# Kernel tuning notes

Hardware: AMD Instinct MI355X
Metric: run time of the kernel (lower is better)

Reference implementation:

```python
import jax, jax.numpy as jnp
import numpy as np

B, T, HID = 2, 1024, 2048
H, DK, DV = 16, 128, 128
KC = 4          # short-conv kernel size
CHUNK = 64
EPS = 1e-5


def _dwconv_silu(x, w):
    # causal depthwise conv1d + SiLU: x [B,T,C], w [C,K]
    K = w.shape[1]
    xp = jnp.pad(x, ((0, 0), (K - 1, 0), (0, 0)))
    y = sum(xp[:, i:i + x.shape[1], :] * w[:, i] for i in range(K))
    return jax.nn.silu(y)


def _l2norm(x):
    return x * jax.lax.rsqrt(jnp.sum(x * x, -1, keepdims=True) + 1e-6)


def setup_inputs() -> dict:
    key = jax.random.key(0)
    ks = jax.random.split(key, 22)
    std = 0.02
    w = lambda k, s: jax.random.normal(k, s, jnp.float32) * std
    return dict(
        hidden_states=jax.random.normal(ks[0], (B, T, HID), jnp.float32),
        Wq=w(ks[1], (HID, H * DK)),
        Wk=w(ks[2], (HID, H * DK)),
        Wv=w(ks[3], (HID, H * DV)),
        conv_wq=w(ks[4], (H * DK, KC)),
        conv_wk=w(ks[5], (H * DK, KC)),
        conv_wv=w(ks[6], (H * DV, KC)),
        Wgb1=w(ks[7], (HID, DV)), Wgb2=w(ks[8], (DV, H * DK)),
        Wgd1=w(ks[9], (HID, DV)), Wgd2=w(ks[10], (DV, H * DK)),
        Wbb=w(ks[11], (HID, H)), Wbd=w(ks[12], (HID, H)),
        Wlam=w(ks[13], (HID, H)),
        A_log=jnp.log(jax.random.uniform(ks[14], (H,), jnp.float32, 1.0, 16.0)),
        dt_bias=jnp.zeros((H * DK,), jnp.float32),
        Wg1=w(ks[15], (HID, DV)), Wg2=w(ks[16], (DV, H * DV)),
        bg2=jnp.zeros((H * DV,), jnp.float32),
        onorm_w=jnp.ones((DV,), jnp.float32),
        Wo=w(ks[17], (H * DV, HID)),
    )


def _fkda_core(q, k, v, gf, gs, bf, bs):
    # dual-state (fast/slow) gated delta rule.
    # q,k: [B,T,H,DK]; v: [B,T,H,DV]; gf/gs: log-decay [B,T,H,DK]; bf/bs: [B,T,H]
    scale = DK ** -0.5
    tm = lambda x: jnp.moveaxis(x, 1, 0)                 # time-major
    qT, kT, vT = tm(q) * scale, tm(k), tm(v)
    g2 = jnp.stack([tm(gf), tm(gs)], 1)                  # [T,2,B,H,DK]
    b2 = jnp.stack([tm(bf), tm(bs)], 1)                  # [T,2,B,H]
    NC = T // CHUNK
    chunkify = lambda x: x.reshape((NC, CHUNK) + x.shape[1:])
    inputs = tuple(map(chunkify, (qT, kT, vT, g2, b2)))

    def step(S, inp):
        qt, kt, vt, gt, bt = inp                         # S: [2,B,H,DK,DV]
        S = S * jnp.exp(gt)[..., None]                   # per-channel decay on key dim
        mem = jnp.einsum('bhk,sbhkv->sbhv', kt, S)       # current memory readout
        u = bt[..., None] * (vt[None] - mem)             # delta-rule residual write
        S = S + jnp.einsum('bhk,sbhv->sbhkv', kt, u)
        o = jnp.einsum('bhk,sbhkv->sbhv', qt, S)
        return S, o

    @jax.checkpoint
    def chunk_step(S, inp):
        return jax.lax.scan(step, S, inp)

    S0 = jnp.zeros((2, q.shape[0], H, DK, DV), q.dtype)
    _, o = jax.lax.scan(chunk_step, S0, inputs)          # [NC,CHUNK,2,B,H,DV]
    o = o.reshape((T,) + o.shape[2:])
    return jnp.moveaxis(o[:, 0], 0, 1), jnp.moveaxis(o[:, 1], 0, 1)


def reference(hidden_states, Wq, Wk, Wv, conv_wq, conv_wk, conv_wv,
              Wgb1, Wgb2, Wgd1, Wgd2, Wbb, Wbd, Wlam, A_log, dt_bias,
              Wg1, Wg2, bg2, onorm_w, Wo):
    x = hidden_states
    b, t, _ = x.shape
    q = _dwconv_silu(x @ Wq, conv_wq).reshape(b, t, H, DK)
    k = _dwconv_silu(x @ Wk, conv_wk).reshape(b, t, H, DK)
    v = _dwconv_silu(x @ Wv, conv_wv).reshape(b, t, H, DV)
    g_base = ((x @ Wgb1) @ Wgb2).reshape(b, t, H, DK)    # low-rank decay gates
    g_delta = ((x @ Wgd1) @ Wgd2).reshape(b, t, H, DK)
    bb, bd = x @ Wbb, x @ Wbd
    lam = jax.nn.sigmoid(x @ Wlam)                       # [b,t,H] fast/slow mix
    beta_fast = jax.nn.sigmoid(bb + bd)
    beta_slow = jax.nn.sigmoid(bb - bd)
    dtb = dt_bias.reshape(H, DK)
    gate_of = lambda g: -jnp.exp(A_log)[None, None, :, None] * jax.nn.softplus(g + dtb)
    gf = gate_of(g_base + g_delta)                       # fused_kda_gate, fast
    gs = gate_of(g_base - g_delta)                       # slow (share_decay_gate=False)
    q, k = _l2norm(q), _l2norm(k)                        # use_qk_l2norm_in_kernel
    o_f, o_s = _fkda_core(q, k, v, gf, gs, beta_fast, beta_slow)
    o = lam[..., None] * o_f + (1.0 - lam[..., None]) * o_s
    gate = ((x @ Wg1) @ Wg2 + bg2).reshape(b, t, H, DV)
    o = o * jax.lax.rsqrt(jnp.mean(o * o, -1, keepdims=True) + EPS) * onorm_w
    o = o * jax.nn.sigmoid(gate)                         # FusedRMSNormGated(sigmoid)
    return o.reshape(b, t, H * DV) @ Wo
```

## Files before the change

### kernel.cpp

```cpp
#include <hip/hip_runtime.h>
#include <hip/hip_bf16.h>
#include <math.h>
#include <stdint.h>

#define B_   2
#define T_   1024
#define HID_ 2048
#define H_   16
#define DK_  128
#define DV_  128
#define TS_  16

typedef __bf16 bf16;
typedef __attribute__((ext_vector_type(8))) __bf16 bf16x8;
typedef __attribute__((ext_vector_type(4))) float f32x4;

typedef __attribute__((address_space(3))) uint32_t* lds_ptr_t;
typedef const __attribute__((address_space(1))) uint32_t* glb_ptr_t;

__device__ __forceinline__ float sigmoidf_(float x) {
    return 1.0f / (1.0f + __expf(-x));
}

__device__ __forceinline__ void ldg_to_lds16(const void* g, void* lds) {
    __builtin_amdgcn_global_load_lds((glb_ptr_t)(uintptr_t)g,
                                     (lds_ptr_t)(uintptr_t)lds, 16, 0, 0);
}

template <int CTRL>
__device__ __forceinline__ float dpp_ror_add(float x) {
    int yi = __builtin_amdgcn_update_dpp(
        0, __builtin_bit_cast(int, x), CTRL, 0xF, 0xF, true);
    return x + __builtin_bit_cast(float, yi);
}
__device__ __forceinline__ float row16_allreduce(float x) {
    x = dpp_ror_add<0x128>(x);
    x = dpp_ror_add<0x124>(x);
    x = dpp_ror_add<0x122>(x);
    x = dpp_ror_add<0x121>(x);
    return x;
}

__global__ __launch_bounds__(256) void cast_bf16_kernel(
    const float* __restrict__ in, bf16* __restrict__ out)
{
    int i = blockIdx.x * 256 + threadIdx.x;
    float4 a = ((const float4*)in)[2 * i];
    float4 b = ((const float4*)in)[2 * i + 1];
    bf16x8 o;
    o[0] = (bf16)a.x; o[1] = (bf16)a.y; o[2] = (bf16)a.z; o[3] = (bf16)a.w;
    o[4] = (bf16)b.x; o[5] = (bf16)b.y; o[6] = (bf16)b.z; o[7] = (bf16)b.w;
    ((bf16x8*)out)[i] = o;
}

__global__ __launch_bounds__(256) void tcast_kernel(
    const float* __restrict__ W, bf16* __restrict__ Wt, int K, int N)
{
    __shared__ float tile[32][33];
    const int k0 = blockIdx.y * 32, n0 = blockIdx.x * 32;
    const int r = threadIdx.x >> 5, c = threadIdx.x & 31;
    #pragma unroll
    for (int i = 0; i < 4; ++i)
        tile[r + 8 * i][c] = W[(size_t)(k0 + r + 8 * i) * N + n0 + c];
    __syncthreads();
    #pragma unroll
    for (int i = 0; i < 4; ++i)
        Wt[(size_t)(n0 + r + 8 * i) * K + k0 + c] = (bf16)tile[c][r + 8 * i];
}

__global__ __launch_bounds__(256) void tcast_off_kernel(
    const float* __restrict__ W, bf16* __restrict__ Wt,
    int N, int noff, int koff, float sign)
{
    __shared__ float tile[32][33];
    const int k0 = blockIdx.y * 32, n0 = blockIdx.x * 32;
    const int r = threadIdx.x >> 5, c = threadIdx.x & 31;
    #pragma unroll
    for (int i = 0; i < 4; ++i)
        tile[r + 8 * i][c] = W[(size_t)(k0 + r + 8 * i) * N + n0 + c];
    __syncthreads();
    #pragma unroll
    for (int i = 0; i < 4; ++i)
        Wt[(size_t)(noff + n0 + r + 8 * i) * 256 + koff + k0 + c] =
            (bf16)(sign * tile[c][r + 8 * i]);
}

__global__ __launch_bounds__(256) void mfma_gemm_kernel(
    const bf16* __restrict__ A, const bf16* __restrict__ Bt,
    const float* __restrict__ bias, void* __restrict__ Cout,
    int M, int N, int Kfull, int lda, int ldc, int bf16out)
{
    __shared__ bf16 As[128 * 32];
    __shared__ bf16 Bs[128 * 32];

    const int tid  = threadIdx.x;
    const int w    = tid >> 6;
    const int lane = tid & 63;
    const int n0   = blockIdx.x * 128;
    const int m0   = blockIdx.y * 128;
    const int wm   = (w >> 1) * 64;
    const int wn   = (w & 1) * 64;

    const int lr = lane >> 2;
    const int lc = (lane & 3) * 8;

    f32x4 acc[4][4];
    #pragma unroll
    for (int i = 0; i < 4; ++i)
        #pragma unroll
        for (int j = 0; j < 4; ++j) acc[i][j] = (f32x4)0.0f;

    const bf16* ApL = As + (wm + (lane & 15)) * 32 + (lane >> 4) * 8;
    const bf16* BpL = Bs + (wn + (lane & 15)) * 32 + (lane >> 4) * 8;

    for (int k0 = 0; k0 < Kfull; k0 += 32) {
        #pragma unroll
        for (int i = 0; i < 2; ++i) {
            const int rr = (w * 2 + i) * 16 + lr;
            ldg_to_lds16(A  + (size_t)(m0 + rr) * lda   + k0 + lc, As + (w * 2 + i) * 512);
            ldg_to_lds16(Bt + (size_t)(n0 + rr) * Kfull + k0 + lc, Bs + (w * 2 + i) * 512);
        }
        __syncthreads();

        bf16x8 af[4], bfr[4];
        #pragma unroll
        for (int i = 0; i < 4; ++i) af[i]  = *(const bf16x8*)(ApL + i * 16 * 32);
        #pragma unroll
        for (int j = 0; j < 4; ++j) bfr[j] = *(const bf16x8*)(BpL + j * 16 * 32);
        #pragma unroll
        for (int i = 0; i < 4; ++i)
            #pragma unroll
            for (int j = 0; j < 4; ++j)
                acc[i][j] = __builtin_amdgcn_mfma_f32_16x16x32_bf16(
                    af[i], bfr[j], acc[i][j], 0, 0, 0);
        __syncthreads();
    }

    #pragma unroll
    for (int i = 0; i < 4; ++i) {
        const int row = m0 + wm + i * 16 + (lane >> 4) * 4;
        #pragma unroll
        for (int j = 0; j < 4; ++j) {
            const int col = n0 + wn + j * 16 + (lane & 15);
            const float bv = bias ? bias[col] : 0.0f;
            #pragma unroll
            for (int r = 0; r < 4; ++r) {
                float v = acc[i][j][r] + bv;
                if (bf16out) ((bf16*)Cout)[(size_t)(row + r) * ldc + col] = (bf16)v;
                else ((float*)Cout)[(size_t)(row + r) * ldc + col] = v;
            }
        }
    }
}

__global__ __launch_bounds__(256) void midcast_kernel(
    const float* __restrict__ src, bf16* __restrict__ midb)
{
    int i = blockIdx.x * 256 + threadIdx.x;
    int m = i / 96, c4 = i - m * 96;
    float4 v = *(const float4*)(src + (size_t)m * 6528 + 6144 + c4 * 4);
    bf16 o[4] = {(bf16)v.x, (bf16)v.y, (bf16)v.z, (bf16)v.w};
    *(uint64_t*)(midb + (size_t)m * 384 + c4 * 4) = *(uint64_t*)o;
}

__global__ __launch_bounds__(256) void skinny3_kernel(
    const float* __restrict__ x, const float* __restrict__ Wbb,
    const float* __restrict__ Wbd, const float* __restrict__ Wlam,
    float* __restrict__ bb, float* __restrict__ bd, float* __restrict__ lam)
{
    __shared__ float xs[16][128];
    __shared__ float wsh[128][48];
    const int m0  = blockIdx.x * 16;
    const int tid = threadIdx.x;
    const int r = tid >> 4, cg = tid & 15;
    float acc0 = 0.f, acc1 = 0.f, acc2 = 0.f;

    for (int k0 = 0; k0 < HID_; k0 += 128) {
        __syncthreads();
        #pragma unroll
        for (int i = 0; i < 2; ++i) {
            int f = tid + 256 * i;
            int rr = f >> 5, cc = (f & 31) * 4;
            *(float4*)&xs[rr][cc] = *(const float4*)(x + (size_t)(m0 + rr) * HID_ + k0 + cc);
        }
        #pragma unroll
        for (int i = 0; i < 2; ++i) {
            int f = tid + 256 * i;
            int kk = f >> 2, cc = (f & 3) * 4;
            *(float4*)&wsh[kk][cc]      = *(const float4*)(Wbb  + (size_t)(k0 + kk) * 16 + cc);
            *(float4*)&wsh[kk][16 + cc] = *(const float4*)(Wbd  + (size_t)(k0 + kk) * 16 + cc);
            *(float4*)&wsh[kk][32 + cc] = *(const float4*)(Wlam + (size_t)(k0 + kk) * 16 + cc);
        }
        __syncthreads();
        #pragma unroll 8
        for (int kk = 0; kk < 128; ++kk) {
            float xv = xs[r][kk];
            acc0 += xv * wsh[kk][cg];
            acc1 += xv * wsh[kk][16 + cg];
            acc2 += xv * wsh[kk][32 + cg];
        }
    }
    size_t o = (size_t)(m0 + r) * 16 + cg;
    bb[o] = acc0; bd[o] = acc1; lam[o] = acc2;
}

__global__ __launch_bounds__(256) void conv_silu_kernel(
    const float* __restrict__ xin, int ldx, int coloff,
    const float* __restrict__ w, float* __restrict__ yout, int mode)
{
    const int bt  = blockIdx.x;
    const int t   = bt & (T_ - 1);
    const int tid = threadIdx.x;
    const float* xr = xin + (size_t)bt * ldx + coloff;

    float val[8];
    #pragma unroll
    for (int jj = 0; jj < 8; ++jj) {
        int c = tid + 256 * jj;
        float4 wc = *(const float4*)(w + (size_t)c * 4);
        const float* xc = xr + c;
        float acc = wc.w * xc[0];
        if (t >= 1) acc += wc.z * xc[-ldx];
        if (t >= 2) acc += wc.y * xc[-2 * ldx];
        if (t >= 3) acc += wc.x * xc[-3 * ldx];
        val[jj] = acc * sigmoidf_(acc);
    }

    if (mode > 0) {
        __shared__ float red[4][8];
        const int wv = tid >> 6;
        #pragma unroll
        for (int jj = 0; jj < 8; ++jj) {
            float v2 = val[jj] * val[jj];
            #pragma unroll
            for (int m = 1; m < 64; m <<= 1) v2 += __shfl_xor(v2, m);
            if ((tid & 63) == 0) red[wv][jj] = v2;
        }
        __syncthreads();
        const int wb = (tid >> 7) * 2;
        #pragma unroll
        for (int jj = 0; jj < 8; ++jj) {
            float ss = red[wb][jj] + red[wb + 1][jj];
            float sc = rsqrtf(ss + 1e-6f);
            if (mode == 2) sc *= 0.08838834764831845f;
            val[jj] *= sc;
        }
    }

    const size_t row = (size_t)bt * HID_;
    #pragma unroll
    for (int jj = 0; jj < 8; ++jj)
        yout[row + tid + 256 * jj] = val[jj];
}

__global__ __launch_bounds__(256) void decay_gate_kernel(
    float* gfgs, const float* __restrict__ A_log,
    const float* __restrict__ dt_bias)
{
    size_t i = (size_t)blockIdx.x * 256 + threadIdx.x;
    int c = (int)(i & (HID_ - 1));
    size_t m = i >> 11;
    int h = c >> 7;
    float* pf = gfgs + m * 4096 + c;
    float* ps = pf + 2048;
    float na = -__expf(A_log[h]);
    float db = dt_bias[c];
    float xf = *pf + db;
    float xs = *ps + db;
    float spf = (xf > 20.0f) ? xf : log1pf(__expf(xf));
    float sps = (xs > 20.0f) ? xs : log1pf(__expf(xs));
    *pf = __expf(na * spf);
    *ps = __expf(na * sps);
}

__global__ __launch_bounds__(256) void fkda_kernel(
    const float* __restrict__ qp, const float* __restrict__ kp,
    const float* __restrict__ vp, const float* __restrict__ egf,
    const float* __restrict__ egs, int ldeg,
    const float* __restrict__ bbp, const float* __restrict__ bdp,
    float* __restrict__ ofp, float* __restrict__ osp)
{
    const int bx = blockIdx.x;
    const int bh = bx & 31;
    const int sv = bx >> 5;
    const int b  = bh >> 4;
    const int h  = bh & 15;
    const int s  = sv >> 3;
    const int vc = sv & 7;

    const float* eg = s ? egs : egf;
    float*       op = s ? osp : ofp;
    const float  bsign = s ? -1.0f : 1.0f;

    const int tid  = threadIdx.x;
    const int lane = tid & 63;
    const int w    = tid >> 6;
    const int kseg = lane & 15;
    const int colb = w * 4 + (lane >> 4);

    const size_t base  = (size_t)b * T_ * HID_ + (size_t)h * DK_;
    const size_t baseg = (size_t)b * T_ * ldeg + (size_t)h * DK_;

    __shared__ float EG[TS_ * 128];
    __shared__ float KK[TS_ * 128];
    __shared__ float QQ[TS_ * 128];
    __shared__ float VV[TS_ * 16];
    __shared__ float OT[TS_ * 16];
    __shared__ float BT[TS_];

    float S[8];
    #pragma unroll
    for (int j = 0; j < 8; ++j) S[j] = 0.0f;

    const int l5  = lane & 31;
    const int ttl = lane >> 5;
    const int cg  = (l5 < 16) ? (l5 * 8) : ((l5 - 16) * 8 + 4);
    const int sl  = kseg * 4;

    for (int t0 = 0; t0 < T_; t0 += TS_) {
        #pragma unroll
        for (int i = 0; i < 2; ++i) {
            int n  = w * 2 + i;
            int tt = n * 2 + ttl;
            size_t rq = base  + (size_t)(t0 + tt) * HID_ + cg;
            size_t rg = baseg + (size_t)(t0 + tt) * ldeg + cg;
            ldg_to_lds16(eg + rg, EG + n * 256);
            ldg_to_lds16(kp + rq, KK + n * 256);
            ldg_to_lds16(qp + rq, QQ + n * 256);
        }
        if (tid < 64) {
            int tt = tid >> 2, vo = (tid & 3) * 4;
            size_t g = base + (size_t)(t0 + tt) * HID_ + vc * 16 + vo;
            ((float4*)VV)[tid] = *(const float4*)(vp + g);
        }
        if (tid < TS_) {
            size_t gi = ((size_t)b * T_ + t0 + tid) * H_ + h;
            BT[tid] = sigmoidf_(bbp[gi] + bsign * bdp[gi]);
        }
        __syncthreads();

        #pragma unroll
        for (int tt = 0; tt < TS_; ++tt) {
            float e[8], kf[8], qf[8];
            *(float4*)&e[0]  = *(const float4*)(EG + tt * 128 + sl);
            *(float4*)&e[4]  = *(const float4*)(EG + tt * 128 + 64 + sl);
            *(float4*)&kf[0] = *(const float4*)(KK + tt * 128 + sl);
            *(float4*)&kf[4] = *(const float4*)(KK + tt * 128 + 64 + sl);
            *(float4*)&qf[0] = *(const float4*)(QQ + tt * 128 + sl);
            *(float4*)&qf[4] = *(const float4*)(QQ + tt * 128 + 64 + sl);
            float vcol = VV[tt * 16 + colb];
            float btv  = BT[tt];

            float p0 = 0.0f, p1 = 0.0f;
            #pragma unroll
            for (int j = 0; j < 8; j += 2) {
                S[j]     *= e[j];     p0 += kf[j]     * S[j];
                S[j + 1] *= e[j + 1]; p1 += kf[j + 1] * S[j + 1];
            }
            float p = row16_allreduce(p0 + p1);

            float u = btv * (vcol - p);

            float o0 = 0.0f, o1 = 0.0f;
            #pragma unroll
            for (int j = 0; j < 8; j += 2) {
                S[j]     += kf[j]     * u; o0 += qf[j]     * S[j];
                S[j + 1] += kf[j + 1] * u; o1 += qf[j + 1] * S[j + 1];
            }
            float oo = row16_allreduce(o0 + o1);

            if (kseg == 0) OT[tt * 16 + colb] = oo;
        }
        __syncthreads();

        if (tid < 64) {
            int tt = tid >> 2, vo = (tid & 3) * 4;
            size_t g = base + (size_t)(t0 + tt) * HID_ + vc * 16 + vo;
            *(float4*)(op + g) = ((const float4*)OT)[tid];
        }
    }
}

__global__ __launch_bounds__(256) void mix_norm_gate_kernel(
    const float* of, const float* os, const float* lam_pre,
    const float* gate, const float* onorm_w, bf16* outp)
{
    const int bt  = blockIdx.x;
    const int tid = threadIdx.x;
    const size_t row = (size_t)bt * HID_;

    float val[8];
    #pragma unroll
    for (int jj = 0; jj < 8; ++jj) {
        int c = tid + 256 * jj;
        int h = c >> 7;
        float l = sigmoidf_(lam_pre[(size_t)bt * H_ + h]);
        val[jj] = l * of[row + c] + (1.0f - l) * os[row + c];
    }

    __shared__ float red[4][8];
    const int wv = tid >> 6;
    #pragma unroll
    for (int jj = 0; jj < 8; ++jj) {
        float v2 = val[jj] * val[jj];
        #pragma unroll
        for (int m = 1; m < 64; m <<= 1) v2 += __shfl_xor(v2, m);
        if ((tid & 63) == 0) red[wv][jj] = v2;
    }
    __syncthreads();
    const int wb = (tid >> 7) * 2;
    #pragma unroll
    for (int jj = 0; jj < 8; ++jj) {
        int c = tid + 256 * jj;
        float ss   = red[wb][jj] + red[wb + 1][jj];
        float mean = ss * (1.0f / 128.0f);
        float sc   = rsqrtf(mean + 1e-5f) * onorm_w[c & 127];
        float g    = sigmoidf_(gate[row + c]);
        outp[row + c] = (bf16)(val[jj] * sc * g);
    }
}

extern "C" void kernel_launch(void* const* d_in, const int* in_sizes, int n_in,
                              void* d_out, int out_size, void* d_ws, size_t ws_size,
                              hipStream_t stream) {
    const float* x       = (const float*)d_in[0];
    const float* Wq      = (const float*)d_in[1];
    const float* Wk      = (const float*)d_in[2];
    const float* Wv      = (const float*)d_in[3];
    const float* conv_wq = (const float*)d_in[4];
    const float* conv_wk = (const float*)d_in[5];
    const float* conv_wv = (const float*)d_in[6];
    const float* Wgb1    = (const float*)d_in[7];
    const float* Wgb2    = (const float*)d_in[8];
    const float* Wgd1    = (const float*)d_in[9];
    const float* Wgd2    = (const float*)d_in[10];
    const float* Wbb     = (const float*)d_in[11];
    const float* Wbd     = (const float*)d_in[12];
    const float* Wlam    = (const float*)d_in[13];
    const float* A_log   = (const float*)d_in[14];
    const float* dt_bias = (const float*)d_in[15];
    const float* Wg1     = (const float*)d_in[16];
    const float* Wg2     = (const float*)d_in[17];
    const float* bg2     = (const float*)d_in[18];
    const float* onorm_w = (const float*)d_in[19];
    const float* Wo      = (const float*)d_in[20];
    float* out = (float*)d_out;

    const size_t M = (size_t)B_ * T_;

    float* ws = (float*)d_ws;
    size_t off = 0;
    auto alloc = [&](size_t nfloats) { float* p = ws + off; off += nfloats; return p; };

    float* bufQKV = alloc(M * 6528);
    float* wqkvTf = alloc((size_t)6528 * HID_ / 2);
    float* xbf    = alloc(M * HID_ / 2);
    float* bufQ   = alloc(M * HID_);
    float* bufK   = alloc(M * HID_);
    float* bufV   = alloc(M * HID_);
    float* bufC   = alloc(M * HID_);
    float* bufD   = alloc(M * HID_);
    float* midbf  = alloc(M * 384 / 2);
    float* bb     = alloc(M * H_);
    float* bd     = alloc(M * H_);
    float* lamp   = alloc(M * H_);

    bf16* xb    = (bf16*)xbf;
    bf16* obf   = (bf16*)xbf;
    bf16* wqkvT = (bf16*)wqkvTf;
    bf16* woT   = wqkvT;
    bf16* wcat  = wqkvT + (size_t)HID_ * HID_;
    bf16* wgate = wcat + (size_t)4096 * 256;
    bf16* midb  = (bf16*)midbf;
    float* gfgs = bufQKV;
    float* bufE = bufQKV + M * 4096;

    dim3 blk(256);
    auto gemm = [&](const bf16* A, const bf16* Bt, const float* bias, void* C,
                    int Mm, int Nn, int Kk, int lda, int ldc, int bf16out) {
        dim3 grid(Nn / 128, Mm / 128);
        mfma_gemm_kernel<<<grid, blk, 0, stream>>>(A, Bt, bias, C, Mm, Nn, Kk,
                                                   lda, ldc, bf16out);
    };
    auto tcast = [&](const float* W, bf16* Wt, int Kk, int Nn) {
        tcast_kernel<<<dim3(Nn / 32, Kk / 32), blk, 0, stream>>>(W, Wt, Kk, Nn);
    };

    cast_bf16_kernel<<<dim3((unsigned)(M * HID_ / 8 / 256)), blk, 0, stream>>>(x, xb);

    tcast(Wq,   wqkvT,                          HID_, HID_);
    tcast(Wk,   wqkvT + (size_t)2048 * HID_,    HID_, HID_);
    tcast(Wv,   wqkvT + (size_t)4096 * HID_,    HID_, HID_);
    tcast(Wgb1, wqkvT + (size_t)6144 * HID_,    HID_, 128);
    tcast(Wgd1, wqkvT + (size_t)6272 * HID_,    HID_, 128);
    tcast(Wg1,  wqkvT + (size_t)6400 * HID_,    HID_, 128);
    gemm(xb, wqkvT, nullptr, bufQKV, (int)M, 6528, HID_, HID_, 6528, 0);

    conv_silu_kernel<<<dim3(B_ * T_), blk, 0, stream>>>(bufQKV, 6528, 0,
        conv_wq, bufQ, 2);
    conv_silu_kernel<<<dim3(B_ * T_), blk, 0, stream>>>(bufQKV, 6528, 2048,
        conv_wk, bufK, 1);
    conv_silu_kernel<<<dim3(B_ * T_), blk, 0, stream>>>(bufQKV, 6528, 4096,
        conv_wv, bufV, 0);

    midcast_kernel<<<dim3((unsigned)(M * 96 / 256)), blk, 0, stream>>>(bufQKV, midb);

    skinny3_kernel<<<dim3((unsigned)(M / 16)), blk, 0, stream>>>(
        x, Wbb, Wbd, Wlam, bb, bd, lamp);

    tcast_off_kernel<<<dim3(64, 4), blk, 0, stream>>>(Wgb2, wcat, HID_, 0,    0,   1.0f);
    tcast_off_kernel<<<dim3(64, 4), blk, 0, stream>>>(Wgd2, wcat, HID_, 0,    128, 1.0f);
    tcast_off_kernel<<<dim3(64, 4), blk, 0, stream>>>(Wgb2, wcat, HID_, 2048, 0,   1.0f);
    tcast_off_kernel<<<dim3(64, 4), blk, 0, stream>>>(Wgd2, wcat, HID_, 2048, 128, -1.0f);
    tcast(Wg2, wgate, 128, HID_);
    tcast(Wo,  woT,   HID_, HID_);
    gemm(midb,       wcat,  nullptr, gfgs, (int)M, 4096, 256, 384, 4096, 0);
    gemm(midb + 256, wgate, bg2,     bufE, (int)M, HID_, 128, 384, HID_, 0);

    decay_gate_kernel<<<dim3((unsigned)(M * HID_ / 256)), blk, 0, stream>>>(
        gfgs, A_log, dt_bias);

    fkda_kernel<<<dim3(512), blk, 0, stream>>>(bufQ, bufK, bufV,
        gfgs, gfgs + 2048, 4096, bb, bd, bufC, bufD);

    mix_norm_gate_kernel<<<dim3(B_ * T_), blk, 0, stream>>>(
        bufC, bufD, lamp, bufE, onorm_w, obf);

    gemm(obf, woT, nullptr, out, (int)M, HID_, HID_, HID_, HID_, 0);
}
```

Measured before the change: 751.1 us.

## Fuse weight casts, conv launches and decay gate; store intermediates in bf16

Merges the many transpose-cast launches into a few batched grids and the three conv launches into one 2D grid. The decay-gate softplus/exp is folded into the GEMM epilogue, and the midcast pass is dropped because the GEMM output is now written as bf16. Q, K and the gate are stored as bf16, and the recurrence kernel loads bf16 Q/K into shared memory. This reduces launch count and memory traffic, at the cost of lower precision for the QKV projection outputs ahead of the conv.

```diff
diff --git a/kernel.cpp b/kernel.cpp
--- a/kernel.cpp
+++ b/kernel.cpp
@@ -53,42 +53,74 @@
     ((bf16x8*)out)[i] = o;
 }
 
-__global__ __launch_bounds__(256) void tcast_kernel(
-    const float* __restrict__ W, bf16* __restrict__ Wt, int K, int N)
-{
+__device__ __forceinline__ void tcast_body(
+    const float* __restrict__ W, bf16* __restrict__ Wt, int K, int N,
+    int bx, int by, float sign)
+{
+    __shared__ float tile[32][33];
+    const int k0 = by * 32, n0 = bx * 32;
+    const int r = threadIdx.x >> 5, c = threadIdx.x & 31;
+    #pragma unroll
+    for (int i = 0; i < 4; ++i)
+        tile[r + 8 * i][c] = W[(size_t)(k0 + r + 8 * i) * N + n0 + c];
+    __syncthreads();
+    #pragma unroll
+    for (int i = 0; i < 4; ++i)
+        Wt[(size_t)(n0 + r + 8 * i) * K + k0 + c] =
+            (bf16)(sign * tile[c][r + 8 * i]);
+}
+
+__global__ __launch_bounds__(256) void tcast4_kernel(
+    const float* Wq, const float* Wk, const float* Wv, const float* Wo,
+    bf16* wqkvT, bf16* woT)
+{
+    const int z = blockIdx.z;
+    const float* src = (z == 0) ? Wq : (z == 1) ? Wk : (z == 2) ? Wv : Wo;
+    bf16* dst = (z < 3) ? (wqkvT + (size_t)z * HID_ * HID_) : woT;
+    tcast_body(src, dst, HID_, HID_, blockIdx.x, blockIdx.y, 1.0f);
+}
+
+__global__ __launch_bounds__(256) void tcast_s3_kernel(
+    const float* Wgb1, const float* Wgd1, const float* Wg1, bf16* wqkvT)
+{
+    const int z = blockIdx.z;
+    const float* src = (z == 0) ? Wgb1 : (z == 1) ? Wgd1 : Wg1;
+    bf16* dst = wqkvT + (size_t)(6144 + z * 128) * HID_;
+    tcast_body(src, dst, HID_, 128, blockIdx.x, blockIdx.y, 1.0f);
+}
+
+__global__ __launch_bounds__(256) void tcast_off4_kernel(
+    const float* Wgb2, const float* Wgd2, bf16* wcat)
+{
+    const int z = blockIdx.z;
+    const float* src = (z & 1) ? Wgd2 : Wgb2;
+    const int noff = (z >= 2) ? 2048 : 0;
+    const int koff = (z & 1) ? 128 : 0;
+    const float sign = (z == 3) ? -1.0f : 1.0f;
     __shared__ float tile[32][33];
     const int k0 = blockIdx.y * 32, n0 = blockIdx.x * 32;
     const int r = threadIdx.x >> 5, c = threadIdx.x & 31;
     #pragma unroll
     for (int i = 0; i < 4; ++i)
-        tile[r + 8 * i][c] = W[(size_t)(k0 + r + 8 * i) * N + n0 + c];
+        tile[r + 8 * i][c] = src[(size_t)(k0 + r + 8 * i) * HID_ + n0 + c];
     __syncthreads();
     #pragma unroll
     for (int i = 0; i < 4; ++i)
-        Wt[(size_t)(n0 + r + 8 * i) * K + k0 + c] = (bf16)tile[c][r + 8 * i];
-}
-
-__global__ __launch_bounds__(256) void tcast_off_kernel(
-    const float* __restrict__ W, bf16* __restrict__ Wt,
-    int N, int noff, int koff, float sign)
-{
-    __shared__ float tile[32][33];
-    const int k0 = blockIdx.y * 32, n0 = blockIdx.x * 32;
-    const int r = threadIdx.x >> 5, c = threadIdx.x & 31;
-    #pragma unroll
-    for (int i = 0; i < 4; ++i)
-        tile[r + 8 * i][c] = W[(size_t)(k0 + r + 8 * i) * N + n0 + c];
-    __syncthreads();
-    #pragma unroll
-    for (int i = 0; i < 4; ++i)
-        Wt[(size_t)(noff + n0 + r + 8 * i) * 256 + koff + k0 + c] =
+        wcat[(size_t)(noff + n0 + r + 8 * i) * 256 + koff + k0 + c] =
             (bf16)(sign * tile[c][r + 8 * i]);
+}
+
+__global__ __launch_bounds__(256) void tcast_g_kernel(
+    const float* Wg2, bf16* wgate)
+{
+    tcast_body(Wg2, wgate, 128, HID_, blockIdx.x, blockIdx.y, 1.0f);
 }
 
 __global__ __launch_bounds__(256) void mfma_gemm_kernel(
     const bf16* __restrict__ A, const bf16* __restrict__ Bt,
     const float* __restrict__ bias, void* __restrict__ Cout,
-    int M, int N, int Kfull, int lda, int ldc, int bf16out)
+    int M, int N, int Kfull, int lda, int ldc, int emode,
+    const float* __restrict__ A_log, const float* __restrict__ dt_bias)
 {
     __shared__ bf16 As[128 * 32];
     __shared__ bf16 Bs[128 * 32];
@@ -142,25 +174,29 @@
         #pragma unroll
         for (int j = 0; j < 4; ++j) {
             const int col = n0 + wn + j * 16 + (lane & 15);
-            const float bv = bias ? bias[col] : 0.0f;
+            float bv = 0.0f, na = 0.0f, db = 0.0f;
+            if (bias) bv = bias[col];
+            if (emode == 2) {
+                int c = col & (HID_ - 1);
+                na = -__expf(A_log[c >> 7]);
+                db = dt_bias[c];
+            }
             #pragma unroll
             for (int r = 0; r < 4; ++r) {
                 float v = acc[i][j][r] + bv;
-                if (bf16out) ((bf16*)Cout)[(size_t)(row + r) * ldc + col] = (bf16)v;
-                else ((float*)Cout)[(size_t)(row + r) * ldc + col] = v;
+                size_t idx = (size_t)(row + r) * ldc + col;
+                if (emode == 0) {
+                    ((float*)Cout)[idx] = v;
+                } else if (emode == 1) {
+                    ((bf16*)Cout)[idx] = (bf16)v;
+                } else {
+                    float xx = v + db;
+                    float sp = (xx > 20.0f) ? xx : log1pf(__expf(xx));
+                    ((float*)Cout)[idx] = __expf(na * sp);
+                }
             }
         }
     }
-}
-
-__global__ __launch_bounds__(256) void midcast_kernel(
-    const float* __restrict__ src, bf16* __restrict__ midb)
-{
-    int i = blockIdx.x * 256 + threadIdx.x;
-    int m = i / 96, c4 = i - m * 96;
-    float4 v = *(const float4*)(src + (size_t)m * 6528 + 6144 + c4 * 4);
-    bf16 o[4] = {(bf16)v.x, (bf16)v.y, (bf16)v.z, (bf16)v.w};
-    *(uint64_t*)(midb + (size_t)m * 384 + c4 * 4) = *(uint64_t*)o;
 }
 
 __global__ __launch_bounds__(256) void skinny3_kernel(
@@ -204,37 +240,41 @@
     bb[o] = acc0; bd[o] = acc1; lam[o] = acc2;
 }
 
-__global__ __launch_bounds__(256) void conv_silu_kernel(
-    const float* __restrict__ xin, int ldx, int coloff,
-    const float* __restrict__ w, float* __restrict__ yout, int mode)
+__global__ __launch_bounds__(256) void conv3_kernel(
+    const bf16* __restrict__ qkvb,
+    const float* __restrict__ wq, const float* __restrict__ wk,
+    const float* __restrict__ wv,
+    bf16* __restrict__ yq, bf16* __restrict__ yk, float* __restrict__ yv)
 {
     const int bt  = blockIdx.x;
+    const int y   = blockIdx.y;
     const int t   = bt & (T_ - 1);
     const int tid = threadIdx.x;
-    const float* xr = xin + (size_t)bt * ldx + coloff;
+    const float* w = (y == 0) ? wq : (y == 1) ? wk : wv;
+    const bf16* xr = qkvb + (size_t)bt * 6528 + y * 2048;
 
     float val[8];
     #pragma unroll
     for (int jj = 0; jj < 8; ++jj) {
         int c = tid + 256 * jj;
         float4 wc = *(const float4*)(w + (size_t)c * 4);
-        const float* xc = xr + c;
-        float acc = wc.w * xc[0];
-        if (t >= 1) acc += wc.z * xc[-ldx];
-        if (t >= 2) acc += wc.y * xc[-2 * ldx];
-        if (t >= 3) acc += wc.x * xc[-3 * ldx];
+        const bf16* xc = xr + c;
+        float acc = wc.w * (float)xc[0];
+        if (t >= 1) acc += wc.z * (float)xc[-6528];
+        if (t >= 2) acc += wc.y * (float)xc[-2 * 6528];
+        if (t >= 3) acc += wc.x * (float)xc[-3 * 6528];
         val[jj] = acc * sigmoidf_(acc);
     }
 
-    if (mode > 0) {
+    if (y < 2) {
         __shared__ float red[4][8];
-        const int wv = tid >> 6;
+        const int wv_ = tid >> 6;
         #pragma unroll
         for (int jj = 0; jj < 8; ++jj) {
             float v2 = val[jj] * val[jj];
             #pragma unroll
             for (int m = 1; m < 64; m <<= 1) v2 += __shfl_xor(v2, m);
-            if ((tid & 63) == 0) red[wv][jj] = v2;
+            if ((tid & 63) == 0) red[wv_][jj] = v2;
         }
         __syncthreads();
         const int wb = (tid >> 7) * 2;
@@ -242,39 +282,24 @@
         for (int jj = 0; jj < 8; ++jj) {
             float ss = red[wb][jj] + red[wb + 1][jj];
             float sc = rsqrtf(ss + 1e-6f);
-            if (mode == 2) sc *= 0.08838834764831845f;
+            if (y == 0) sc *= 0.08838834764831845f;
             val[jj] *= sc;
         }
-    }
-
-    const size_t row = (size_t)bt * HID_;
-    #pragma unroll
-    for (int jj = 0; jj < 8; ++jj)
-        yout[row + tid + 256 * jj] = val[jj];
-}
-
-__global__ __launch_bounds__(256) void decay_gate_kernel(
-    float* gfgs, const float* __restrict__ A_log,
-    const float* __restrict__ dt_bias)
-{
-    size_t i = (size_t)blockIdx.x * 256 + threadIdx.x;
-    int c = (int)(i & (HID_ - 1));
-    size_t m = i >> 11;
-    int h = c >> 7;
-    float* pf = gfgs + m * 4096 + c;
-    float* ps = pf + 2048;
-    float na = -__expf(A_log[h]);
-    float db = dt_bias[c];
-    float xf = *pf + db;
-    float xs = *ps + db;
-    float spf = (xf > 20.0f) ? xf : log1pf(__expf(xf));
-    float sps = (xs > 20.0f) ? xs : log1pf(__expf(xs));
-    *pf = __expf(na * spf);
-    *ps = __expf(na * sps);
+        bf16* yo = (y == 0) ? yq : yk;
+        const size_t row = (size_t)bt * HID_;
+        #pragma unroll
+        for (int jj = 0; jj < 8; ++jj)
+            yo[row + tid + 256 * jj] = (bf16)val[jj];
+    } else {
+        const size_t row = (size_t)bt * HID_;
+        #pragma unroll
+        for (int jj = 0; jj < 8; ++jj)
+            yv[row + tid + 256 * jj] = val[jj];
+    }
 }
 
 __global__ __launch_bounds__(256) void fkda_kernel(
-    const float* __restrict__ qp, const float* __restrict__ kp,
+    const bf16* __restrict__ qp, const bf16* __restrict__ kp,
     const float* __restrict__ vp, const float* __restrict__ egf,
     const float* __restrict__ egs, int ldeg,
     const float* __restrict__ bbp, const float* __restrict__ bdp,
@@ -302,8 +327,8 @@
     const size_t baseg = (size_t)b * T_ * ldeg + (size_t)h * DK_;
 
     __shared__ float EG[TS_ * 128];
-    __shared__ float KK[TS_ * 128];
-    __shared__ float QQ[TS_ * 128];
+    __shared__ bf16  KK[TS_ * 128];
+    __shared__ bf16  QQ[TS_ * 128];
     __shared__ float VV[TS_ * 16];
     __shared__ float OT[TS_ * 16];
     __shared__ float BT[TS_];
@@ -317,16 +342,20 @@
     const int cg  = (l5 < 16) ? (l5 * 8) : ((l5 - 16) * 8 + 4);
     const int sl  = kseg * 4;
 
+    const int krow = w * 4 + (lane >> 4);
+    const int kcol = (lane & 15) * 8;
+
     for (int t0 = 0; t0 < T_; t0 += TS_) {
         #pragma unroll
         for (int i = 0; i < 2; ++i) {
             int n  = w * 2 + i;
             int tt = n * 2 + ttl;
-            size_t rq = base  + (size_t)(t0 + tt) * HID_ + cg;
-            size_t rg = baseg + (size_t)(t0 + tt) * ldeg + cg;
-            ldg_to_lds16(eg + rg, EG + n * 256);
-            ldg_to_lds16(kp + rq, KK + n * 256);
-            ldg_to_lds16(qp + rq, QQ + n * 256);
+            ldg_to_lds16(eg + baseg + (size_t)(t0 + tt) * ldeg + cg, EG + n * 256);
+        }
+        {
+            size_t g = base + (size_t)(t0 + krow) * HID_ + kcol;
+            ldg_to_lds16(kp + g, KK + w * 512);
+            ldg_to_lds16(qp + g, QQ + w * 512);
         }
         if (tid < 64) {
             int tt = tid >> 2, vo = (tid & 3) * 4;
@@ -341,15 +370,17 @@
 
         #pragma unroll
         for (int tt = 0; tt < TS_; ++tt) {
-            float e[8], kf[8], qf[8];
-            *(float4*)&e[0]  = *(const float4*)(EG + tt * 128 + sl);
-            *(float4*)&e[4]  = *(const float4*)(EG + tt * 128 + 64 + sl);
-            *(float4*)&kf[0] = *(const float4*)(KK + tt * 128 + sl);
-            *(float4*)&kf[4] = *(const float4*)(KK + tt * 128 + 64 + sl);
-            *(float4*)&qf[0] = *(const float4*)(QQ + tt * 128 + sl);
-            *(float4*)&qf[4] = *(const float4*)(QQ + tt * 128 + 64 + sl);
+            float e[8];
+            *(float4*)&e[0] = *(const float4*)(EG + tt * 128 + sl);
+            *(float4*)&e[4] = *(const float4*)(EG + tt * 128 + 64 + sl);
+            bf16x8 k8 = *(const bf16x8*)(KK + tt * 128 + kseg * 8);
+            bf16x8 q8 = *(const bf16x8*)(QQ + tt * 128 + kseg * 8);
             float vcol = VV[tt * 16 + colb];
             float btv  = BT[tt];
+
+            float kf[8], qf[8];
+            #pragma unroll
+            for (int j = 0; j < 8; ++j) { kf[j] = (float)k8[j]; qf[j] = (float)q8[j]; }
 
             float p0 = 0.0f, p1 = 0.0f;
             #pragma unroll
@@ -383,7 +414,7 @@
 
 __global__ __launch_bounds__(256) void mix_norm_gate_kernel(
     const float* of, const float* os, const float* lam_pre,
-    const float* gate, const float* onorm_w, bf16* outp)
+    const bf16* gate, const float* onorm_w, bf16* outp)
 {
     const int bt  = blockIdx.x;
     const int tid = threadIdx.x;
@@ -415,7 +446,7 @@
         float ss   = red[wb][jj] + red[wb + 1][jj];
         float mean = ss * (1.0f / 128.0f);
         float sc   = rsqrtf(mean + 1e-5f) * onorm_w[c & 127];
-        float g    = sigmoidf_(gate[row + c]);
+        float g    = sigmoidf_((float)gate[row + c]);
         outp[row + c] = (bf16)(val[jj] * sc * g);
     }
 }
@@ -452,73 +483,64 @@
     size_t off = 0;
     auto alloc = [&](size_t nfloats) { float* p = ws + off; off += nfloats; return p; };
 
-    float* bufQKV = alloc(M * 6528);
+    float* xbf    = alloc(M * HID_ / 2);
+    float* qkvbf  = alloc(M * 6528 / 2);
     float* wqkvTf = alloc((size_t)6528 * HID_ / 2);
-    float* xbf    = alloc(M * HID_ / 2);
-    float* bufQ   = alloc(M * HID_);
-    float* bufK   = alloc(M * HID_);
+    float* woTf   = alloc((size_t)HID_ * HID_ / 2);
+    float* wcatf  = alloc((size_t)4096 * 256 / 2);
+    float* wgatef = alloc((size_t)HID_ * 128 / 2);
+    float* bufQf  = alloc(M * HID_ / 2);
+    float* bufKf  = alloc(M * HID_ / 2);
     float* bufV   = alloc(M * HID_);
+    float* gfgs   = alloc(M * 4096);
+    float* bufEf  = alloc(M * HID_ / 2);
     float* bufC   = alloc(M * HID_);
     float* bufD   = alloc(M * HID_);
-    float* midbf  = alloc(M * 384 / 2);
     float* bb     = alloc(M * H_);
     float* bd     = alloc(M * H_);
     float* lamp   = alloc(M * H_);
 
     bf16* xb    = (bf16*)xbf;
     bf16* obf   = (bf16*)xbf;
+    bf16* qkvb  = (bf16*)qkvbf;
     bf16* wqkvT = (bf16*)wqkvTf;
-    bf16* woT   = wqkvT;
-    bf16* wcat  = wqkvT + (size_t)HID_ * HID_;
-    bf16* wgate = wcat + (size_t)4096 * 256;
-    bf16* midb  = (bf16*)midbf;
-    float* gfgs = bufQKV;
-    float* bufE = bufQKV + M * 4096;
+    bf16* woT   = (bf16*)woTf;
+    bf16* wcat  = (bf16*)wcatf;
+    bf16* wgate = (bf16*)wgatef;
+    bf16* bufQ  = (bf16*)bufQf;
+    bf16* bufK  = (bf16*)bufKf;
+    bf16* bufE  = (bf16*)bufEf;
 
     dim3 blk(256);
     auto gemm = [&](const bf16* A, const bf16* Bt, const float* bias, void* C,
-                    int Mm, int Nn, int Kk, int lda, int ldc, int bf16out) {
+                    int Mm, int Nn, int Kk, int lda, int ldc, int emode,
+                    const float* a1, const float* a2) {
         dim3 grid(Nn / 128, Mm / 128);
         mfma_gemm_kernel<<<grid, blk, 0, stream>>>(A, Bt, bias, C, Mm, Nn, Kk,
-                                                   lda, ldc, bf16out);
+                                                   lda, ldc, emode, a1, a2);
     };
-    auto tcast = [&](const float* W, bf16* Wt, int Kk, int Nn) {
-        tcast_kernel<<<dim3(Nn / 32, Kk / 32), blk, 0, stream>>>(W, Wt, Kk, Nn);
-    };
 
     cast_bf16_kernel<<<dim3((unsigned)(M * HID_ / 8 / 256)), blk, 0, stream>>>(x, xb);
 
-    tcast(Wq,   wqkvT,                          HID_, HID_);
-    tcast(Wk,   wqkvT + (size_t)2048 * HID_,    HID_, HID_);
-    tcast(Wv,   wqkvT + (size_t)4096 * HID_,    HID_, HID_);
-    tcast(Wgb1, wqkvT + (size_t)6144 * HID_,    HID_, 128);
-    tcast(Wgd1, wqkvT + (size_t)6272 * HID_,    HID_, 128);
-    tcast(Wg1,  wqkvT + (size_t)6400 * HID_,    HID_, 128);
-    gemm(xb, wqkvT, nullptr, bufQKV, (int)M, 6528, HID_, HID_, 6528, 0);
-
-    conv_silu_kernel<<<dim3(B_ * T_), blk, 0, stream>>>(bufQKV, 6528, 0,
-        conv_wq, bufQ, 2);
-    conv_silu_kernel<<<dim3(B_ * T_), blk, 0, stream>>>(bufQKV, 6528, 2048,
-        conv_wk, bufK, 1);
-    conv_silu_kernel<<<dim3(B_ * T_), blk, 0, stream>>>(bufQKV, 6528, 4096,
-        conv_wv, bufV, 0);
-
-    midcast_kernel<<<dim3((unsigned)(M * 96 / 256)), blk, 0, stream>>>(bufQKV, midb);
+    tcast4_kernel<<<dim3(64, 64, 4), blk, 0, stream>>>(Wq, Wk, Wv, Wo, wqkvT, woT);
+    tcast_s3_kernel<<<dim3(4, 64, 3), blk, 0, stream>>>(Wgb1, Wgd1, Wg1, wqkvT);
+    tcast_off4_kernel<<<dim3(64, 4, 4), blk, 0, stream>>>(Wgb2, Wgd2, wcat);
+    tcast_g_kernel<<<dim3(64, 4), blk, 0, stream>>>(Wg2, wgate);
+
+    gemm(xb, wqkvT, nullptr, qkvb, (int)M, 6528, HID_, HID_, 6528, 1,
+         nullptr, nullptr);
+
+    conv3_kernel<<<dim3(B_ * T_, 3), blk, 0, stream>>>(
+        qkvb, conv_wq, conv_wk, conv_wv, bufQ, bufK, bufV);
 
     skinny3_kernel<<<dim3((unsigned)(M / 16)), blk, 0, stream>>>(
         x, Wbb, Wbd, Wlam, bb, bd, lamp);
 
-    tcast_off_kernel<<<dim3(64, 4), blk, 0, stream>>>(Wgb2, wcat, HID_, 0,    0,   1.0f);
-    tcast_off_kernel<<<dim3(64, 4), blk, 0, stream>>>(Wgd2, wcat, HID_, 0,    128, 1.0f);
-    tcast_off_kernel<<<dim3(64, 4), blk, 0, stream>>>(Wgb2, wcat, HID_, 2048, 0,   1.0f);
-    tcast_off_kernel<<<dim3(64, 4), blk, 0, stream>>>(Wgd2, wcat, HID_, 2048, 128, -1.0f);
-    tcast(Wg2, wgate, 128, HID_);
-    tcast(Wo,  woT,   HID_, HID_);
-    gemm(midb,       wcat,  nullptr, gfgs, (int)M, 4096, 256, 384, 4096, 0);
-    gemm(midb + 256, wgate, bg2,     bufE, (int)M, HID_, 128, 384, HID_, 0);
-
-    decay_gate_kernel<<<dim3((unsigned)(M * HID_ / 256)), blk, 0, stream>>>(
-        gfgs, A_log, dt_bias);
+    gemm(qkvb + 6144, wcat, nullptr, gfgs, (int)M, 4096, 256, 6528, 4096, 2,
+         A_log, dt_bias);
+
+    gemm(qkvb + 6400, wgate, bg2, bufE, (int)M, HID_, 128, 6528, HID_, 1,
+         nullptr, nullptr);
 
     fkda_kernel<<<dim3(512), blk, 0, stream>>>(bufQ, bufK, bufV,
         gfgs, gfgs + 2048, 4096, bb, bd, bufC, bufD);
@@ -526,5 +548,6 @@
     mix_norm_gate_kernel<<<dim3(B_ * T_), blk, 0, stream>>>(
         bufC, bufD, lamp, bufE, onorm_w, obf);
 
-    gemm(obf, woT, nullptr, out, (int)M, HID_, HID_, HID_, HID_, 0);
-}
+    gemm(obf, woT, nullptr, out, (int)M, HID_, HID_, HID_, HID_, 0,
+         nullptr, nullptr);
+}
```

Result: slower. 769.7 us (+2.5%).
